# Kernel optimization log

Hardware: AMD Instinct MI355X
Metric: run time of the kernel (lower is better)

The kernel has to match this reference:

```python
import jax, jax.numpy as jnp
import numpy as np

N_HEADS = 4
HEAD_DIM = 64
NEG_SLOPE = 0.2
TIME_PE_DIM = 16


def time_pe(date):
    # TimePositionalEncoding: sin/cos features; 8 sin + 8 cos == pe_dim (16), no projection needed
    t = date.astype(jnp.float32) / 10000.0
    div = jnp.exp(jnp.arange(0, TIME_PE_DIM, 2, dtype=jnp.float32) * (-jnp.log(10000.0) / TIME_PE_DIM))
    arg = t[:, None] * div[None, :]  # [N, 8]
    return jnp.concatenate([jnp.sin(arg), jnp.cos(arg)], axis=-1)  # [N, 16]


def pearl_pe(x, edge_index, Wp, bp):
    # PEARL positional embedding approximated as mean-neighbor aggregation over the
    # union of all relations followed by a learned linear + tanh -> [N, 32]
    N = x.shape[0]
    src = edge_index[:, 0, :].reshape(-1)
    dst = edge_index[:, 1, :].reshape(-1)
    agg = jax.ops.segment_sum(x[src], dst, num_segments=N)
    deg = jax.ops.segment_sum(jnp.ones_like(dst, jnp.float32), dst, num_segments=N)
    agg = agg / jnp.maximum(deg, 1.0)[:, None]
    return jnp.tanh(agg @ Wp + bp)


def gatv2(x, src, dst, Wl, Wr, att, b):
    # GATv2 message passing for one edge type; dropout is identity (eval mode)
    N = x.shape[0]
    xl = (x @ Wl).reshape(N, N_HEADS, HEAD_DIM)
    xr = (x @ Wr).reshape(N, N_HEADS, HEAD_DIM)
    m = xl[src] + xr[dst]                                   # [E, H, C]
    e = jnp.sum(jax.nn.leaky_relu(m, NEG_SLOPE) * att, -1)  # [E, H]
    emax = jax.ops.segment_max(e, dst, num_segments=N)
    emax = jnp.where(jnp.isfinite(emax), emax, 0.0)
    ex = jnp.exp(e - emax[dst])
    denom = jax.ops.segment_sum(ex, dst, num_segments=N)
    alpha = ex / (denom[dst] + 1e-16)                       # segment softmax over in-edges
    out = jax.ops.segment_sum(xl[src] * alpha[..., None], dst, num_segments=N)
    return out.reshape(N, N_HEADS * HEAD_DIM) + b


def rel_agg(h_rel, W, b, a):
    # attention-weighted combination across relation outputs: h_rel [N, R, hidden]
    s = jnp.einsum('nrh,h->nr', jnp.tanh(h_rel @ W + b), a)
    w = jax.nn.softmax(s, axis=-1)
    return jnp.einsum('nr,nrh->nh', w, h_rel)


def gnn_layer(h, edge_index, Wl, Wr, att, b, aW, ab, aa):
    R = edge_index.shape[0]
    # HeteroConv aggr='sum': sum GATv2 outputs across the 5 relations
    conv_sum = gatv2(h, edge_index[0, 0], edge_index[0, 1], Wl[0], Wr[0], att[0], b[0])
    for r in range(1, R):
        conv_sum = conv_sum + gatv2(h, edge_index[r, 0], edge_index[r, 1], Wl[r], Wr[r], att[r], b[r])
    # original forward feeds conv_output['stock'] for every relation key (identical copies)
    h_rel = jnp.broadcast_to(conv_sum[:, None, :], (conv_sum.shape[0], R, conv_sum.shape[1]))
    h = rel_agg(h_rel, aW, ab, aa)
    return jax.nn.relu(h)  # dropout identity in eval


def reference(x, date_tensor, edge_index, pearl_W, pearl_b, Wl0, Wr0, att0, b0,
              Wl1, Wr1, att1, b1, aggW, aggb, agga, out_W1, out_b1, out_W2, out_b2):
    pe = pearl_pe(x, edge_index, pearl_W, pearl_b)          # [N, 32]
    tpe = time_pe(date_tensor)                              # [N, 16]
    h = jnp.concatenate([x, pe, tpe], axis=1)               # [N, 112]
    h = gnn_layer(h, edge_index, Wl0, Wr0, att0, b0, aggW[0], aggb[0], agga[0])
    h = gnn_layer(h, edge_index, Wl1, Wr1, att1, b1, aggW[1], aggb[1], agga[1])
    h = jax.nn.relu(h @ out_W1 + out_b1)
    return h @ out_W2 + out_b2                              # [N, 3]


def setup_inputs():
    key = jax.random.key(0)
    ks = jax.random.split(key, 20)
    N, E, R = 20000, 320000, 5
    IN, PE, HID = 64, 32, 256
    IN0 = IN + PE + TIME_PE_DIM  # 112

    def nrm(k, shp, sc=0.05):
        return jax.random.normal(k, shp, jnp.float32) * sc

    return {
        'x': jax.random.normal(ks[0], (N, IN), jnp.float32),
        'date_tensor': jax.random.randint(ks[1], (N,), 0, 20000, jnp.int32),
        'edge_index': jax.random.randint(ks[2], (R, 2, E), 0, N, jnp.int32),
        'pearl_W': nrm(ks[3], (IN, PE)),
        'pearl_b': jnp.zeros((PE,), jnp.float32),
        'Wl0': nrm(ks[4], (R, IN0, HID)),
        'Wr0': nrm(ks[5], (R, IN0, HID)),
        'att0': nrm(ks[6], (R, N_HEADS, HEAD_DIM)),
        'b0': jnp.zeros((R, HID), jnp.float32),
        'Wl1': nrm(ks[7], (R, HID, HID)),
        'Wr1': nrm(ks[8], (R, HID, HID)),
        'att1': nrm(ks[9], (R, N_HEADS, HEAD_DIM)),
        'b1': jnp.zeros((R, HID), jnp.float32),
        'aggW': nrm(ks[10], (2, HID, HID)),
        'aggb': jnp.zeros((2, HID), jnp.float32),
        'agga': nrm(ks[11], (2, HID)),
        'out_W1': nrm(ks[12], (HID, HID // 2)),
        'out_b1': jnp.zeros((HID // 2,), jnp.float32),
        'out_W2': nrm(ks[13], (HID // 2, 3)),
        'out_b2': jnp.zeros((3,), jnp.float32),
    }
```

## Files before the change

kernel.cpp:

```cpp
#include <hip/hip_runtime.h>
#include <math.h>

typedef __bf16 bf16x8 __attribute__((ext_vector_type(8)));
typedef float f32x4 __attribute__((ext_vector_type(4)));
typedef unsigned short u16x8 __attribute__((ext_vector_type(8)));

#define GLD16(src, dst)                                                        \
    __builtin_amdgcn_global_load_lds(                                          \
        (const __attribute__((address_space(1))) void*)(src),                  \
        (__attribute__((address_space(3))) void*)(dst), 16, 0, 0)

__device__ inline float bf2f(unsigned short u) {
    union { unsigned int i; float f; } c;
    c.i = ((unsigned int)u) << 16;
    return c.f;
}


__global__ __launch_bounds__(256) void count_kernel(const int* __restrict__ ei,
                                                    int* __restrict__ cnt, int N, int E) {
    int idx = blockIdx.x * 256 + threadIdx.x;
    if (idx >= 5 * E) return;
    int r = idx / E;
    int e = idx - r * E;
    int dst = ei[(size_t)r * 2 * E + E + e];
    atomicAdd(&cnt[r * N + dst], 1);
}

__global__ __launch_bounds__(256) void scanA_kernel(const int* __restrict__ cnt,
                                                    int* __restrict__ off,
                                                    int* __restrict__ csums, int N, int NC) {
    int r = blockIdx.y, c = blockIdx.x, t = threadIdx.x;
    int idx0 = c * 1024 + t * 4;
    int v0 = (idx0 + 0 < N) ? cnt[r * N + idx0 + 0] : 0;
    int v1 = (idx0 + 1 < N) ? cnt[r * N + idx0 + 1] : 0;
    int v2 = (idx0 + 2 < N) ? cnt[r * N + idx0 + 2] : 0;
    int v3 = (idx0 + 3 < N) ? cnt[r * N + idx0 + 3] : 0;
    int ts = v0 + v1 + v2 + v3;
    __shared__ int sd[256];
    sd[t] = ts;
    __syncthreads();
    for (int s = 1; s < 256; s <<= 1) {
        int add = (t >= s) ? sd[t - s] : 0;
        __syncthreads();
        sd[t] += add;
        __syncthreads();
    }
    int excl = sd[t] - ts;
    size_t base = (size_t)r * (N + 1);
    if (idx0 + 0 < N) off[base + idx0 + 0] = excl;
    if (idx0 + 1 < N) off[base + idx0 + 1] = excl + v0;
    if (idx0 + 2 < N) off[base + idx0 + 2] = excl + v0 + v1;
    if (idx0 + 3 < N) off[base + idx0 + 3] = excl + v0 + v1 + v2;
    if (t == 255) csums[r * NC + c] = sd[255];
}

__global__ __launch_bounds__(64) void scanB_kernel(int* __restrict__ csums,
                                                   int* __restrict__ off, int N, int NC) {
    int r = threadIdx.x;
    if (r < 5) {
        int run = 0;
        for (int c = 0; c < NC; c++) {
            int t = csums[r * NC + c];
            csums[r * NC + c] = run;
            run += t;
        }
        off[(size_t)r * (N + 1) + N] = run;
    }
}

__global__ __launch_bounds__(256) void scanC_kernel(int* __restrict__ off,
                                                    const int* __restrict__ csums,
                                                    int N, int NC) {
    int r = blockIdx.y, c = blockIdx.x, t = threadIdx.x;
    int add = csums[r * NC + c];
    int idx0 = c * 1024 + t * 4;
    size_t base = (size_t)r * (N + 1);
#pragma unroll
    for (int j = 0; j < 4; j++)
        if (idx0 + j < N) off[base + idx0 + j] += add;
}

__global__ __launch_bounds__(256) void scatter_kernel(const int* __restrict__ ei,
                                                      const int* __restrict__ off,
                                                      int* __restrict__ cur,
                                                      unsigned short* __restrict__ srcs,
                                                      int N, int E) {
    int idx = blockIdx.x * 256 + threadIdx.x;
    if (idx >= 5 * E) return;
    int r = idx / E;
    int e = idx - r * E;
    int src = ei[(size_t)r * 2 * E + e];
    int dst = ei[(size_t)r * 2 * E + E + e];
    int pos = atomicAdd(&cur[r * N + dst], 1);
    srcs[(size_t)r * E + off[(size_t)r * (N + 1) + dst] + pos] = (unsigned short)src;
}


__global__ __launch_bounds__(256) void xcvt_kernel(const float* __restrict__ x,
                                                   unsigned short* __restrict__ xb, int total) {
    int idx = (blockIdx.x * 256 + threadIdx.x) * 4;
    if (idx >= total) return;
    float4 v = *(const float4*)(x + idx);
    __bf16 b0 = (__bf16)v.x, b1 = (__bf16)v.y, b2 = (__bf16)v.z, b3 = (__bf16)v.w;
    unsigned short* p = xb + idx;
    p[0] = *(unsigned short*)&b0;
    p[1] = *(unsigned short*)&b1;
    p[2] = *(unsigned short*)&b2;
    p[3] = *(unsigned short*)&b3;
}


__global__ __launch_bounds__(256) void pearl_h0_kernel(
    const float* __restrict__ x, const unsigned short* __restrict__ xb,
    const int* __restrict__ date,
    const int* __restrict__ off, const unsigned short* __restrict__ srcs,
    const float* __restrict__ pW, const float* __restrict__ pb,
    float* __restrict__ h0, int N, int E) {
    int lane = threadIdx.x & 63;
    int wid = blockIdx.x * 4 + (threadIdx.x >> 6);
    if (wid >= N) return;
    int n = __builtin_amdgcn_readfirstlane(wid);

    float acc = 0.f;
    int deg = 0;
    for (int r = 0; r < 5; r++) {
        int kb = off[(size_t)r * (N + 1) + n];
        int ke = off[(size_t)r * (N + 1) + n + 1];
        deg += ke - kb;
        const unsigned short* sp = srcs + (size_t)r * E;
        int k = kb;
        for (; k + 8 <= ke; k += 8) {
            int i0 = sp[k], i1 = sp[k + 1], i2 = sp[k + 2], i3 = sp[k + 3];
            int i4 = sp[k + 4], i5 = sp[k + 5], i6 = sp[k + 6], i7 = sp[k + 7];
            float a0 = bf2f(xb[(size_t)i0 * 64 + lane]);
            float a1 = bf2f(xb[(size_t)i1 * 64 + lane]);
            float a2 = bf2f(xb[(size_t)i2 * 64 + lane]);
            float a3 = bf2f(xb[(size_t)i3 * 64 + lane]);
            float a4 = bf2f(xb[(size_t)i4 * 64 + lane]);
            float a5 = bf2f(xb[(size_t)i5 * 64 + lane]);
            float a6 = bf2f(xb[(size_t)i6 * 64 + lane]);
            float a7 = bf2f(xb[(size_t)i7 * 64 + lane]);
            acc += ((a0 + a1) + (a2 + a3)) + ((a4 + a5) + (a6 + a7));
        }
        for (; k < ke; k++) acc += bf2f(xb[(size_t)sp[k] * 64 + lane]);
    }
    float an = acc / fmaxf((float)deg, 1.0f);

    float s = (lane < 32) ? pb[lane] : 0.f;
#pragma unroll 8
    for (int c = 0; c < 64; c++) {
        float av = __shfl(an, c, 64);
        if (lane < 32) s = fmaf(av, pW[c * 32 + lane], s);
    }

    h0[(size_t)n * 112 + lane] = x[(size_t)n * 64 + lane];
    if (lane < 32) h0[(size_t)n * 112 + 64 + lane] = tanhf(s);
    if (lane < 16) {
        float t = (float)date[n] / 10000.0f;
        int i = lane & 7;
        float dv = expf((float)(2 * i) * (-0.57564627324851148f));
        float arg = t * dv;
        h0[(size_t)n * 112 + 96 + lane] = (lane < 8) ? sinf(arg) : cosf(arg);
    }
}


__global__ __launch_bounds__(256) void pack_a_kernel(
    const float* __restrict__ A, __bf16* __restrict__ Ah, __bf16* __restrict__ Al,
    int M, int K, int Mp, int KT) {
    int KG = KT * 4;
    int idx = blockIdx.x * 256 + threadIdx.x;
    if (idx >= Mp * KG) return;
    int m = idx / KG, kgg = idx - m * KG;
    int kt = kgg >> 2, kg = kgg & 3;
    int k0 = kt * 32 + kg * 8;
    int mt = m >> 4, mr = m & 15;
    size_t out = (((size_t)mt * KT + kt) * 64 + kg * 16 + mr) * 8;
    bf16x8 hv, lv;
#pragma unroll
    for (int j = 0; j < 8; j++) {
        int k = k0 + j;
        float v = (m < M && k < K) ? A[(size_t)m * K + k] : 0.f;
        __bf16 h = (__bf16)v;
        hv[j] = h;
        lv[j] = (__bf16)(v - (float)h);
    }
    *(bf16x8*)(Ah + out) = hv;
    *(bf16x8*)(Al + out) = lv;
}


__global__ __launch_bounds__(256) void pack_w_kernel(
    const float* __restrict__ Wl0, const float* __restrict__ Wr0,
    const float* __restrict__ Wl1, const float* __restrict__ Wr1,
    const float* __restrict__ W1,
    __bf16* __restrict__ Wph, __bf16* __restrict__ Wpl) {
    const int S0 = 32768, S1 = 65536;
    int t = blockIdx.y;
    const float* W;
    int K, Nc, KT;
    size_t dst;
    if (t < 5)       { W = Wl0 + (size_t)t * 112 * 256;        K = 112; Nc = 256; KT = 4; dst = (size_t)t * S0; }
    else if (t < 10) { W = Wr0 + (size_t)(t - 5) * 112 * 256;  K = 112; Nc = 256; KT = 4; dst = 163840 + (size_t)(t - 5) * S0; }
    else if (t < 15) { W = Wl1 + (size_t)(t - 10) * 256 * 256; K = 256; Nc = 256; KT = 8; dst = 327680 + (size_t)(t - 10) * S1; }
    else if (t < 20) { W = Wr1 + (size_t)(t - 15) * 256 * 256; K = 256; Nc = 256; KT = 8; dst = 655360 + (size_t)(t - 15) * S1; }
    else             { W = W1;                                  K = 256; Nc = 128; KT = 8; dst = 983040; }
    int entries = (Nc / 16) * KT * 64;
    int idx = blockIdx.x * 256 + threadIdx.x;
    if (idx >= entries) return;
    int nt = idx / (KT * 64);
    int rem = idx - nt * (KT * 64);
    int kt = rem >> 6, lane = rem & 63;
    int kg = lane >> 4, nr = lane & 15;
    bf16x8 hv, lv;
#pragma unroll
    for (int j = 0; j < 8; j++) {
        int k = kt * 32 + kg * 8 + j;
        float v = (k < K) ? W[(size_t)k * Nc + nt * 16 + nr] : 0.f;
        __bf16 h = (__bf16)v;
        hv[j] = h;
        lv[j] = (__bf16)(v - (float)h);
    }
    *(bf16x8*)(Wph + dst + (size_t)idx * 8) = hv;
    *(bf16x8*)(Wpl + dst + (size_t)idx * 8) = lv;
}


__global__ __launch_bounds__(256) void gemm_mfma(
    const __bf16* __restrict__ Ah, const __bf16* __restrict__ Al,
    const __bf16* __restrict__ WLh, const __bf16* __restrict__ WLl,
    const __bf16* __restrict__ WRh, const __bf16* __restrict__ WRl,
    size_t strideB, void* __restrict__ Cl, void* __restrict__ Cr, size_t CstrideBytes,
    int M, int Nout, int KT, const float* __restrict__ bias, int do_relu,
    int npL, int npR, int out_bf16, int NYT, int per_bx) {
    int lin = blockIdx.x;
    int bx = lin / per_bx, rem = lin % per_bx;
    int by = rem % NYT; rem /= NYT;
    int side = rem & 1;
    int r = rem >> 1;

    const __bf16* Bh = (side ? WRh : WLh) + (size_t)r * strideB;
    const __bf16* Bl = (side ? WRl : WLl) + (size_t)r * strideB;
    char* C = (char*)(side ? Cr : Cl) + (size_t)r * CstrideBytes;
    int np = side ? npR : npL;

    __shared__ __bf16 sAh[8 * 512], sAl[8 * 512], sBh[8 * 512], sBl[8 * 512];

    int tid = threadIdx.x, lane = tid & 63, w = tid >> 6;
    int wr = w >> 1, wc = w & 1;

    f32x4 acc[4][4] = {};

    for (int kt = 0; kt < KT; ++kt) {
        int tl = w * 2;
        size_t a0 = ((size_t)(bx * 8 + tl) * KT + kt) * 512 + lane * 8;
        size_t a1 = ((size_t)(bx * 8 + tl + 1) * KT + kt) * 512 + lane * 8;
        size_t b0 = ((size_t)(by * 8 + tl) * KT + kt) * 512 + lane * 8;
        size_t b1 = ((size_t)(by * 8 + tl + 1) * KT + kt) * 512 + lane * 8;
        GLD16(Ah + a0, sAh + tl * 512);
        GLD16(Ah + a1, sAh + (tl + 1) * 512);
        GLD16(Bh + b0, sBh + tl * 512);
        GLD16(Bh + b1, sBh + (tl + 1) * 512);
        if (np >= 2) {
            GLD16(Al + a0, sAl + tl * 512);
            GLD16(Al + a1, sAl + (tl + 1) * 512);
        }
        if (np == 3) {
            GLD16(Bl + b0, sBl + tl * 512);
            GLD16(Bl + b1, sBl + (tl + 1) * 512);
        }
        __syncthreads();

        bf16x8 ah[4], al[4], bh[4], bl[4];
#pragma unroll
        for (int i = 0; i < 4; i++) {
            ah[i] = *(const bf16x8*)(sAh + (wr * 4 + i) * 512 + lane * 8);
            bh[i] = *(const bf16x8*)(sBh + (wc * 4 + i) * 512 + lane * 8);
        }
        if (np >= 2) {
#pragma unroll
            for (int i = 0; i < 4; i++)
                al[i] = *(const bf16x8*)(sAl + (wr * 4 + i) * 512 + lane * 8);
        }
        if (np == 3) {
#pragma unroll
            for (int i = 0; i < 4; i++)
                bl[i] = *(const bf16x8*)(sBl + (wc * 4 + i) * 512 + lane * 8);
        }
#pragma unroll
        for (int i = 0; i < 4; i++)
#pragma unroll
            for (int j = 0; j < 4; j++) {
                acc[i][j] = __builtin_amdgcn_mfma_f32_16x16x32_bf16(ah[i], bh[j], acc[i][j], 0, 0, 0);
                if (np >= 2)
                    acc[i][j] = __builtin_amdgcn_mfma_f32_16x16x32_bf16(al[i], bh[j], acc[i][j], 0, 0, 0);
                if (np == 3)
                    acc[i][j] = __builtin_amdgcn_mfma_f32_16x16x32_bf16(ah[i], bl[j], acc[i][j], 0, 0, 0);
            }
        __syncthreads();
    }

    int rb = bx * 128 + wr * 64, cb = by * 128 + wc * 64;
#pragma unroll
    for (int i = 0; i < 4; i++) {
#pragma unroll
        for (int j = 0; j < 4; j++) {
            int row0 = rb + i * 16 + (lane >> 4) * 4;
            int col = cb + j * 16 + (lane & 15);
            float bv = bias ? bias[col] : 0.f;
#pragma unroll
            for (int q = 0; q < 4; q++) {
                int row = row0 + q;
                if (row < M) {
                    float v = acc[i][j][q] + bv;
                    if (do_relu) v = fmaxf(v, 0.f);
                    if (out_bf16)
                        ((__bf16*)C)[(size_t)row * Nout + col] = (__bf16)v;
                    else
                        ((float*)C)[(size_t)row * Nout + col] = v;
                }
            }
        }
    }
}


__global__ __launch_bounds__(256) void gat5_kernel(
    const unsigned short* __restrict__ xl5, const unsigned short* __restrict__ xr5,
    const float* __restrict__ att,
    const int* __restrict__ csrOff,
    const unsigned short* __restrict__ csrSrc,
    float* __restrict__ conv, const float* __restrict__ bvec,
    int N, int E, int do_relu) {
    int lane = threadIdx.x & 63;
    int wid = blockIdx.x * 4 + (threadIdx.x >> 6);
    if (wid >= N) return;
    int n = __builtin_amdgcn_readfirstlane(wid);
    int e = lane >> 4;
    int sub = lane & 15;
    int cb = (sub >> 2) * 64 + (sub & 3) * 16;
    int wc = cb + e * 4;

    float4 cv = {0.f, 0.f, 0.f, 0.f};
#pragma unroll
    for (int r = 0; r < 5; r++) {
        float4 b = *(const float4*)(bvec + r * 256 + wc);
        cv.x += b.x; cv.y += b.y; cv.z += b.z; cv.w += b.w;
    }

    for (int r = 0; r < 5; r++) {
        const unsigned short* xl = xl5 + (size_t)r * N * 256;
        float rv[16], av[16];
        {
            const unsigned short* xrp = xr5 + ((size_t)r * N + n) * 256 + cb;
            u16x8 q0 = *(const u16x8*)(xrp);
            u16x8 q1 = *(const u16x8*)(xrp + 8);
#pragma unroll
            for (int j = 0; j < 8; j++) { rv[j] = bf2f(q0[j]); rv[8 + j] = bf2f(q1[j]); }
#pragma unroll
            for (int j = 0; j < 16; j += 4) {
                float4 a = *(const float4*)(att + r * 256 + cb + j);
                av[j] = a.x; av[j + 1] = a.y; av[j + 2] = a.z; av[j + 3] = a.w;
            }
        }

        float m = -3.0e38f, d = 0.f;
        float A[16];
#pragma unroll
        for (int j = 0; j < 16; j++) A[j] = 0.f;

        const int* off = csrOff + (size_t)r * (N + 1);
        const unsigned short* sp = csrSrc + (size_t)r * E;
        int kb = off[n], ke = off[n + 1];
        if (kb < ke) {
            int kl = ke - 1;
            int ki = kb + e;
            int s = sp[(ki <= kl) ? ki : kl];
            float c[16];
            {
                const unsigned short* xp = xl + (size_t)s * 256 + cb;
                u16x8 q0 = *(const u16x8*)(xp);
                u16x8 q1 = *(const u16x8*)(xp + 8);
#pragma unroll
                for (int j = 0; j < 8; j++) { c[j] = bf2f(q0[j]); c[8 + j] = bf2f(q1[j]); }
            }
            for (int k = kb; k < ke; k += 4) {
                int kn = k + 4 + e;
                int sn = sp[(kn <= kl) ? kn : kl];
                const unsigned short* np_ = xl + (size_t)sn * 256 + cb;
                u16x8 n0 = *(const u16x8*)(np_);
                u16x8 n1 = *(const u16x8*)(np_ + 8);

                float p = 0.f;
#pragma unroll
                for (int j = 0; j < 16; j++) {
                    float t = c[j] + rv[j];
                    t = (t > 0.f) ? t : 0.2f * t;
                    p = fmaf(t, av[j], p);
                }
                p += __shfl_xor(p, 1, 64);
                p += __shfl_xor(p, 2, 64);
                bool valid = (k + e) < ke;
                if (!valid) p = -3.0e38f;

                if (__any(p > m)) {
                    float nm = fmaxf(m, p);
                    float sc = __expf(m - nm);
                    d *= sc;
#pragma unroll
                    for (int j = 0; j < 16; j++) A[j] *= sc;
                    m = nm;
                }
                float wg = valid ? __expf(p - m) : 0.f;
                d += wg;
#pragma unroll
                for (int j = 0; j < 16; j++) A[j] = fmaf(wg, c[j], A[j]);

#pragma unroll
                for (int j = 0; j < 8; j++) { c[j] = bf2f(n0[j]); c[8 + j] = bf2f(n1[j]); }
            }
        }

        float M = fmaxf(m, __shfl_xor(m, 16, 64));
        M = fmaxf(M, __shfl_xor(M, 32, 64));
        float sc = __expf(m - M);
        d *= sc;
        d += __shfl_xor(d, 16, 64);
        d += __shfl_xor(d, 32, 64);
#pragma unroll
        for (int j = 0; j < 16; j++) {
            A[j] *= sc;
            A[j] += __shfl_xor(A[j], 16, 64);
            A[j] += __shfl_xor(A[j], 32, 64);
        }

        float inv = 1.0f / (d + 1e-16f);
        cv.x = fmaf(A[e * 4 + 0], inv, cv.x);
        cv.y = fmaf(A[e * 4 + 1], inv, cv.y);
        cv.z = fmaf(A[e * 4 + 2], inv, cv.z);
        cv.w = fmaf(A[e * 4 + 3], inv, cv.w);
    }

    if (do_relu) {
        cv.x = fmaxf(cv.x, 0.f);
        cv.y = fmaxf(cv.y, 0.f);
        cv.z = fmaxf(cv.z, 0.f);
        cv.w = fmaxf(cv.w, 0.f);
    }
    *(float4*)(conv + (size_t)n * 256 + wc) = cv;
}


__global__ __launch_bounds__(256) void head_kernel(const float* __restrict__ hm,
                                                   const float* __restrict__ W2,
                                                   const float* __restrict__ b2,
                                                   float* __restrict__ out, int N) {
    int lane = threadIdx.x & 63;
    int wid = blockIdx.x * 4 + (threadIdx.x >> 6);
    if (wid >= N) return;
    int n = __builtin_amdgcn_readfirstlane(wid);
    float a0 = hm[(size_t)n * 128 + lane];
    float a1 = hm[(size_t)n * 128 + 64 + lane];
    float s0 = a0 * W2[lane * 3 + 0] + a1 * W2[(64 + lane) * 3 + 0];
    float s1 = a0 * W2[lane * 3 + 1] + a1 * W2[(64 + lane) * 3 + 1];
    float s2 = a0 * W2[lane * 3 + 2] + a1 * W2[(64 + lane) * 3 + 2];
#pragma unroll
    for (int sft = 1; sft < 64; sft <<= 1) {
        s0 += __shfl_xor(s0, sft, 64);
        s1 += __shfl_xor(s1, sft, 64);
        s2 += __shfl_xor(s2, sft, 64);
    }
    if (lane == 0) {
        out[(size_t)n * 3 + 0] = s0 + b2[0];
        out[(size_t)n * 3 + 1] = s1 + b2[1];
        out[(size_t)n * 3 + 2] = s2 + b2[2];
    }
}


extern "C" void kernel_launch(void* const* d_in, const int* in_sizes, int n_in,
                              void* d_out, int out_size, void* d_ws, size_t ws_size,
                              hipStream_t stream) {
    const float* x    = (const float*)d_in[0];
    const int* date   = (const int*)d_in[1];
    const int* ei     = (const int*)d_in[2];
    const float* pW   = (const float*)d_in[3];
    const float* pb   = (const float*)d_in[4];
    const float* Wl0  = (const float*)d_in[5];
    const float* Wr0  = (const float*)d_in[6];
    const float* att0 = (const float*)d_in[7];
    const float* b0   = (const float*)d_in[8];
    const float* Wl1  = (const float*)d_in[9];
    const float* Wr1  = (const float*)d_in[10];
    const float* att1 = (const float*)d_in[11];
    const float* b1   = (const float*)d_in[12];
    const float* outW1 = (const float*)d_in[16];
    const float* outb1 = (const float*)d_in[17];
    const float* outW2 = (const float*)d_in[18];
    const float* outb2 = (const float*)d_in[19];
    float* out = (float*)d_out;

    int N = in_sizes[0] / 64;
    int E = in_sizes[2] / 10;
    int Mp = ((N + 127) / 128) * 128;
    int MT = Mp / 128;
    int NC = (N + 1023) / 1024;

    char* ws = (char*)d_ws;
    size_t o = 0;
    auto alloc = [&](size_t bytes) -> char* {
        char* p = ws + o;
        o += (bytes + 255) & ~(size_t)255;
        return p;
    };
    int* cur               = (int*)alloc((size_t)5 * N * 4);
    int* csrOff            = (int*)alloc((size_t)5 * (N + 1) * 4);
    unsigned short* csrSrc = (unsigned short*)alloc((size_t)5 * E * 2);
    int* csums             = (int*)alloc((size_t)5 * NC * 4);
    unsigned short* xb16   = (unsigned short*)alloc((size_t)N * 64 * 2);
    float* h0              = (float*)alloc((size_t)N * 112 * 4);
    float* conv            = (float*)alloc((size_t)N * 256 * 4);
    unsigned short* xl5    = (unsigned short*)alloc((size_t)5 * N * 256 * 2);
    unsigned short* xr5    = (unsigned short*)alloc((size_t)5 * N * 256 * 2);
    __bf16* Aph            = (__bf16*)alloc((size_t)Mp * 256 * 2);
    __bf16* Apl            = (__bf16*)alloc((size_t)Mp * 256 * 2);
    __bf16* Wph            = (__bf16*)alloc((size_t)1015808 * 2);
    __bf16* Wpl            = (__bf16*)alloc((size_t)1015808 * 2);
    float* hmid            = (float*)xl5;
    (void)ws_size;

    const size_t S0 = 32768, S1 = 65536;
    const size_t oWl0 = 0, oWr0 = 163840, oWl1 = 327680, oWr1 = 655360, oW1 = 983040;
    size_t xstride = (size_t)N * 256 * 2;

    int totE = 5 * E;

    hipMemsetAsync(cur, 0, (size_t)5 * N * 4, stream);
    count_kernel<<<(totE + 255) / 256, 256, 0, stream>>>(ei, cur, N, E);
    scanA_kernel<<<dim3(NC, 5), 256, 0, stream>>>(cur, csrOff, csums, N, NC);
    scanB_kernel<<<1, 64, 0, stream>>>(csums, csrOff, N, NC);
    scanC_kernel<<<dim3(NC, 5), 256, 0, stream>>>(csrOff, csums, N, NC);
    hipMemsetAsync(cur, 0, (size_t)5 * N * 4, stream);
    scatter_kernel<<<(totE + 255) / 256, 256, 0, stream>>>(ei, csrOff, cur, csrSrc, N, E);

    xcvt_kernel<<<(N * 64 / 4 + 255) / 256, 256, 0, stream>>>(x, xb16, N * 64);
    pearl_h0_kernel<<<(N + 3) / 4, 256, 0, stream>>>(x, xb16, date, csrOff, csrSrc, pW, pb, h0, N, E);

    pack_w_kernel<<<dim3(32, 21, 1), 256, 0, stream>>>(Wl0, Wr0, Wl1, Wr1, outW1, Wph, Wpl);

    pack_a_kernel<<<(Mp * 16 + 255) / 256, 256, 0, stream>>>(h0, Aph, Apl, N, 112, Mp, 4);
    gemm_mfma<<<MT * 20, 256, 0, stream>>>(
        Aph, Apl, Wph + oWl0, Wpl + oWl0, Wph + oWr0, Wpl + oWr0, S0,
        xl5, xr5, xstride, N, 256, 4, nullptr, 0, 2, 1, 1, 2, 20);
    gat5_kernel<<<(N + 3) / 4, 256, 0, stream>>>(xl5, xr5, att0, csrOff, csrSrc,
                                                 conv, b0, N, E, 1);

    pack_a_kernel<<<(Mp * 32 + 255) / 256, 256, 0, stream>>>(conv, Aph, Apl, N, 256, Mp, 8);
    gemm_mfma<<<MT * 20, 256, 0, stream>>>(
        Aph, Apl, Wph + oWl1, Wpl + oWl1, Wph + oWr1, Wpl + oWr1, S1,
        xl5, xr5, xstride, N, 256, 8, nullptr, 0, 2, 1, 1, 2, 20);
    gat5_kernel<<<(N + 3) / 4, 256, 0, stream>>>(xl5, xr5, att1, csrOff, csrSrc,
                                                 conv, b1, N, E, 1);

    pack_a_kernel<<<(Mp * 32 + 255) / 256, 256, 0, stream>>>(conv, Aph, Apl, N, 256, Mp, 8);
    gemm_mfma<<<MT, 256, 0, stream>>>(
        Aph, Apl, Wph + oW1, Wpl + oW1, Wph + oW1, Wpl + oW1, 0,
        hmid, hmid, 0, N, 128, 8, outb1, 1, 3, 3, 0, 1, 1);
    head_kernel<<<(N + 3) / 4, 256, 0, stream>>>(hmid, outW2, outb2, out, N);
}
```

Baseline: 786.4 us.

## Fuse GAT output packing into gat5, seed scatter cursors from scan, widen pearl gather

The GAT aggregation kernel now writes its ReLU output directly as split hi/lo bf16 in the tiled layout the MFMA GEMM expects. This removes the fp32 conv buffer and both pack_a launches for layers 1 and 2. The CSR build seeds the scatter cursors with the prefix offsets in scanC, which drops a memset and an offset load per edge in scatter. The PEARL neighbour gather is unrolled to 16 loads per step to expose more memory-level parallelism. The risk is that the hand-computed packed index must exactly match the pack_a layout, and the wider unroll raises register use.

```diff
diff --git a/kernel.cpp b/kernel.cpp
--- a/kernel.cpp
+++ b/kernel.cpp
@@ -2,6 +2,7 @@
 #include <math.h>
 
 typedef __bf16 bf16x8 __attribute__((ext_vector_type(8)));
+typedef __bf16 bf16x4 __attribute__((ext_vector_type(4)));
 typedef float f32x4 __attribute__((ext_vector_type(4)));
 typedef unsigned short u16x8 __attribute__((ext_vector_type(8)));
 
@@ -71,6 +72,7 @@
 
 __global__ __launch_bounds__(256) void scanC_kernel(int* __restrict__ off,
                                                     const int* __restrict__ csums,
+                                                    int* __restrict__ cur,
                                                     int N, int NC) {
     int r = blockIdx.y, c = blockIdx.x, t = threadIdx.x;
     int add = csums[r * NC + c];
@@ -78,11 +80,14 @@
     size_t base = (size_t)r * (N + 1);
 #pragma unroll
     for (int j = 0; j < 4; j++)
-        if (idx0 + j < N) off[base + idx0 + j] += add;
+        if (idx0 + j < N) {
+            int v = off[base + idx0 + j] + add;
+            off[base + idx0 + j] = v;
+            cur[r * N + idx0 + j] = v;
+        }
 }
 
 __global__ __launch_bounds__(256) void scatter_kernel(const int* __restrict__ ei,
-                                                      const int* __restrict__ off,
                                                       int* __restrict__ cur,
                                                       unsigned short* __restrict__ srcs,
                                                       int N, int E) {
@@ -93,7 +98,7 @@
     int src = ei[(size_t)r * 2 * E + e];
     int dst = ei[(size_t)r * 2 * E + E + e];
     int pos = atomicAdd(&cur[r * N + dst], 1);
-    srcs[(size_t)r * E + off[(size_t)r * (N + 1) + dst] + pos] = (unsigned short)src;
+    srcs[(size_t)r * E + pos] = (unsigned short)src;
 }
 
 
@@ -130,18 +135,24 @@
         deg += ke - kb;
         const unsigned short* sp = srcs + (size_t)r * E;
         int k = kb;
-        for (; k + 8 <= ke; k += 8) {
+        for (; k + 16 <= ke; k += 16) {
+            int ix[16];
+#pragma unroll
+            for (int j = 0; j < 16; j++) ix[j] = sp[k + j];
+            float a[16];
+#pragma unroll
+            for (int j = 0; j < 16; j++) a[j] = bf2f(xb[(size_t)ix[j] * 64 + lane]);
+            float s0 = ((a[0] + a[1]) + (a[2] + a[3])) + ((a[4] + a[5]) + (a[6] + a[7]));
+            float s1 = ((a[8] + a[9]) + (a[10] + a[11])) + ((a[12] + a[13]) + (a[14] + a[15]));
+            acc += s0 + s1;
+        }
+        for (; k + 4 <= ke; k += 4) {
             int i0 = sp[k], i1 = sp[k + 1], i2 = sp[k + 2], i3 = sp[k + 3];
-            int i4 = sp[k + 4], i5 = sp[k + 5], i6 = sp[k + 6], i7 = sp[k + 7];
             float a0 = bf2f(xb[(size_t)i0 * 64 + lane]);
             float a1 = bf2f(xb[(size_t)i1 * 64 + lane]);
             float a2 = bf2f(xb[(size_t)i2 * 64 + lane]);
             float a3 = bf2f(xb[(size_t)i3 * 64 + lane]);
-            float a4 = bf2f(xb[(size_t)i4 * 64 + lane]);
-            float a5 = bf2f(xb[(size_t)i5 * 64 + lane]);
-            float a6 = bf2f(xb[(size_t)i6 * 64 + lane]);
-            float a7 = bf2f(xb[(size_t)i7 * 64 + lane]);
-            acc += ((a0 + a1) + (a2 + a3)) + ((a4 + a5) + (a6 + a7));
+            acc += (a0 + a1) + (a2 + a3);
         }
         for (; k < ke; k++) acc += bf2f(xb[(size_t)sp[k] * 64 + lane]);
     }
@@ -331,8 +342,9 @@
     const float* __restrict__ att,
     const int* __restrict__ csrOff,
     const unsigned short* __restrict__ csrSrc,
-    float* __restrict__ conv, const float* __restrict__ bvec,
-    int N, int E, int do_relu) {
+    __bf16* __restrict__ Ah, __bf16* __restrict__ Al,
+    const float* __restrict__ bvec,
+    int N, int E) {
     int lane = threadIdx.x & 63;
     int wid = blockIdx.x * 4 + (threadIdx.x >> 6);
     if (wid >= N) return;
@@ -442,13 +454,21 @@
         cv.w = fmaf(A[e * 4 + 3], inv, cv.w);
     }
 
-    if (do_relu) {
-        cv.x = fmaxf(cv.x, 0.f);
-        cv.y = fmaxf(cv.y, 0.f);
-        cv.z = fmaxf(cv.z, 0.f);
-        cv.w = fmaxf(cv.w, 0.f);
-    }
-    *(float4*)(conv + (size_t)n * 256 + wc) = cv;
+    cv.x = fmaxf(cv.x, 0.f);
+    cv.y = fmaxf(cv.y, 0.f);
+    cv.z = fmaxf(cv.z, 0.f);
+    cv.w = fmaxf(cv.w, 0.f);
+    float vv[4] = {cv.x, cv.y, cv.z, cv.w};
+    bf16x4 hv, lv;
+#pragma unroll
+    for (int j = 0; j < 4; j++) {
+        __bf16 h = (__bf16)vv[j];
+        hv[j] = h;
+        lv[j] = (__bf16)(vv[j] - (float)h);
+    }
+    size_t outp = (((size_t)(n >> 4) * 8 + (wc >> 5)) * 64 + ((wc >> 3) & 3) * 16 + (n & 15)) * 8 + (wc & 7);
+    *(bf16x4*)(Ah + outp) = hv;
+    *(bf16x4*)(Al + outp) = lv;
 }
 
 
@@ -520,7 +540,6 @@
     int* csums             = (int*)alloc((size_t)5 * NC * 4);
     unsigned short* xb16   = (unsigned short*)alloc((size_t)N * 64 * 2);
     float* h0              = (float*)alloc((size_t)N * 112 * 4);
-    float* conv            = (float*)alloc((size_t)N * 256 * 4);
     unsigned short* xl5    = (unsigned short*)alloc((size_t)5 * N * 256 * 2);
     unsigned short* xr5    = (unsigned short*)alloc((size_t)5 * N * 256 * 2);
     __bf16* Aph            = (__bf16*)alloc((size_t)Mp * 256 * 2);
@@ -540,9 +559,8 @@
     count_kernel<<<(totE + 255) / 256, 256, 0, stream>>>(ei, cur, N, E);
     scanA_kernel<<<dim3(NC, 5), 256, 0, stream>>>(cur, csrOff, csums, N, NC);
     scanB_kernel<<<1, 64, 0, stream>>>(csums, csrOff, N, NC);
-    scanC_kernel<<<dim3(NC, 5), 256, 0, stream>>>(csrOff, csums, N, NC);
-    hipMemsetAsync(cur, 0, (size_t)5 * N * 4, stream);
-    scatter_kernel<<<(totE + 255) / 256, 256, 0, stream>>>(ei, csrOff, cur, csrSrc, N, E);
+    scanC_kernel<<<dim3(NC, 5), 256, 0, stream>>>(csrOff, csums, cur, N, NC);
+    scatter_kernel<<<(totE + 255) / 256, 256, 0, stream>>>(ei, cur, csrSrc, N, E);
 
     xcvt_kernel<<<(N * 64 / 4 + 255) / 256, 256, 0, stream>>>(x, xb16, N * 64);
     pearl_h0_kernel<<<(N + 3) / 4, 256, 0, stream>>>(x, xb16, date, csrOff, csrSrc, pW, pb, h0, N, E);
@@ -554,16 +572,14 @@
         Aph, Apl, Wph + oWl0, Wpl + oWl0, Wph + oWr0, Wpl + oWr0, S0,
         xl5, xr5, xstride, N, 256, 4, nullptr, 0, 2, 1, 1, 2, 20);
     gat5_kernel<<<(N + 3) / 4, 256, 0, stream>>>(xl5, xr5, att0, csrOff, csrSrc,
-                                                 conv, b0, N, E, 1);
-
-    pack_a_kernel<<<(Mp * 32 + 255) / 256, 256, 0, stream>>>(conv, Aph, Apl, N, 256, Mp, 8);
+                                                 Aph, Apl, b0, N, E);
+
     gemm_mfma<<<MT * 20, 256, 0, stream>>>(
         Aph, Apl, Wph + oWl1, Wpl + oWl1, Wph + oWr1, Wpl + oWr1, S1,
         xl5, xr5, xstride, N, 256, 8, nullptr, 0, 2, 1, 1, 2, 20);
     gat5_kernel<<<(N + 3) / 4, 256, 0, stream>>>(xl5, xr5, att1, csrOff, csrSrc,
-                                                 conv, b1, N, E, 1);
-
-    pack_a_kernel<<<(Mp * 32 + 255) / 256, 256, 0, stream>>>(conv, Aph, Apl, N, 256, Mp, 8);
+                                                 Aph, Apl, b1, N, E);
+
     gemm_mfma<<<MT, 256, 0, stream>>>(
         Aph, Apl, Wph + oW1, Wpl + oW1, Wph + oW1, Wpl + oW1, 0,
         hmid, hmid, 0, N, 128, 8, outb1, 1, 3, 3, 0, 1, 1);
```

New measurement: 755.5 us. -3.9%, faster.
